# Performance work log

Hardware: AMD Instinct MI355X
Metric: run time of the kernel (lower is better)

Reference implementation:

```python
import jax, jax.numpy as jnp
import numpy as np

K = 3  # n_neighbors


def setup_inputs() -> dict:
    key = jax.random.key(0)
    k1, k2, k3 = jax.random.split(key, 3)
    N, D, C, B = 400000, 27, 11, 512  # train size, 3*N_PEAKS_MAX, classes, query batch
    train_features = jax.random.normal(k1, (N, D), dtype=jnp.float32)
    label_idx = jax.random.randint(k2, (N,), 0, C)
    train_labels = jax.nn.one_hot(label_idx, C, dtype=jnp.float32)
    query = jax.random.normal(k3, (B, D), dtype=jnp.float32)
    return {"query": query, "train_features": train_features, "train_labels": train_labels}


def _divide_no_nan(x, y):
    # tf.math.divide_no_nan: 0 where denominator is 0
    y_safe = jnp.where(y != 0, y, 1.0)
    return jnp.where(y != 0, x / y_safe, 0.0)


def reference(query, train_features, train_labels):
    # scale = per-feature max abs over training set (computed in __init__)
    scale = jnp.max(jnp.abs(train_features), axis=0)            # [D]
    train_s = _divide_no_nan(train_features, scale)             # [N,D]
    q_s = _divide_no_nan(query, scale)                          # [B,D]

    xn = jnp.sum(train_s * train_s, axis=1)                     # [N]
    qn = jnp.sum(q_s * q_s, axis=1)                             # [B]
    d2 = qn[:, None] - 2.0 * jnp.einsum('bd,nd->bn', q_s, train_s) + xn[None, :]
    dist = jnp.sqrt(jnp.maximum(d2, 0.0))                       # [B,N]

    neg_kd, idx = jax.lax.top_k(-dist, K)                       # k smallest distances
    kd = -neg_kd                                                # [B,K]

    lab = train_labels[idx]                                     # [B,K,C]
    # inverse-distance weighted vote (safe against zero distances)
    kd_safe = jnp.where(kd == 0.0, 1.0, kd)
    votes = jnp.sum(lab / kd_safe[:, :, None], axis=1)          # [B,C]
    vote_res = jax.nn.one_hot(jnp.argmax(votes, axis=1), train_labels.shape[1], dtype=jnp.float32)

    # exact-match branch: if the nearest distance is 0, return its label directly
    zero_hit = (jnp.min(kd, axis=1) == 0.0)[:, None]            # [B,1]
    result = jnp.where(zero_hit, lab[:, 0, :], vote_res)        # [B,C]
    return kd, result
```

## Files before the change

### kernel.cpp

```cpp
#include <hip/hip_runtime.h>
#include <math.h>

typedef _Float16 h8 __attribute__((ext_vector_type(8)));
typedef float    f4v __attribute__((ext_vector_type(4)));

#define N_TRAIN 400000
#define DIMS    27
#define BQ      512
#define NCLS    11
#define KNN     3
#define NB      500
#define P1T     1024
#define PTS_BLK 800
#define PTS_SUP 160
#define NSUP    5
#define NPT     10
#define RAWF    4320
#define TILE_B  2048
#define NC      (NB * KNN)
#define SCB     391
#define P2T     512

#define U64MAX 0xFFFFFFFFFFFFFFFFULL

__global__ __launch_bounds__(256) void k_scale(const float* __restrict__ train,
                                               unsigned* __restrict__ scale_u) {
    __shared__ float red[4][DIMS];
    int tid = threadIdx.x;
    int lane = tid & 63, w = tid >> 6;
    int g = blockIdx.x * 256 + tid;
    float m[DIMS];
#pragma unroll
    for (int d = 0; d < DIMS; ++d) m[d] = 0.f;
    if (g < N_TRAIN / 4) {
        const uint4* p = (const uint4*)(train + (size_t)g * (4 * DIMS));
#pragma unroll
        for (int k = 0; k < DIMS; ++k) {
            uint4 v = p[k];
            m[(4 * k + 0) % DIMS] = fmaxf(m[(4 * k + 0) % DIMS], fabsf(__uint_as_float(v.x)));
            m[(4 * k + 1) % DIMS] = fmaxf(m[(4 * k + 1) % DIMS], fabsf(__uint_as_float(v.y)));
            m[(4 * k + 2) % DIMS] = fmaxf(m[(4 * k + 2) % DIMS], fabsf(__uint_as_float(v.z)));
            m[(4 * k + 3) % DIMS] = fmaxf(m[(4 * k + 3) % DIMS], fabsf(__uint_as_float(v.w)));
        }
    }
#pragma unroll
    for (int d = 0; d < DIMS; ++d) {
        float t = m[d];
#pragma unroll
        for (int st = 1; st < 64; st <<= 1) t = fmaxf(t, __shfl_xor(t, st, 64));
        m[d] = t;
    }
    if (lane == 0) {
#pragma unroll
        for (int d = 0; d < DIMS; ++d) red[w][d] = m[d];
    }
    __syncthreads();
    if (tid < DIMS) {
        float v = fmaxf(fmaxf(red[0][tid], red[1][tid]), fmaxf(red[2][tid], red[3][tid]));
        atomicMax(&scale_u[tid], __float_as_uint(v));
    }
}

__device__ __forceinline__ void insert3(float d, int i, float* bd, int* bi) {
    if (d < bd[2] || (d == bd[2] && i < bi[2])) {
        if (d < bd[1] || (d == bd[1] && i < bi[1])) {
            bd[2] = bd[1]; bi[2] = bi[1];
            if (d < bd[0] || (d == bd[0] && i < bi[0])) {
                bd[1] = bd[0]; bi[1] = bi[0];
                bd[0] = d; bi[0] = i;
            } else { bd[1] = d; bi[1] = i; }
        } else { bd[2] = d; bi[2] = i; }
    }
}

__device__ __forceinline__ unsigned long long shfl_xor_u64(unsigned long long v, int m) {
    unsigned lo = (unsigned)v, hi = (unsigned)(v >> 32);
    lo = __shfl_xor(lo, m, 64);
    hi = __shfl_xor(hi, m, 64);
    return ((unsigned long long)hi << 32) | lo;
}

__device__ __forceinline__ void ins3u64(unsigned long long e,
                                        unsigned long long& t0,
                                        unsigned long long& t1,
                                        unsigned long long& t2) {
    unsigned long long a  = e < t2 ? e : t2;
    unsigned long long n2 = t1 > a ? t1 : a;
    unsigned long long n1 = t1 < a ? t1 : a;
    t2 = n2;
    unsigned long long m1 = t0 > n1 ? t0 : n1;
    t0 = t0 < n1 ? t0 : n1;
    t1 = m1;
}

__device__ __forceinline__ void stage16(const float* g, float* l) {
    __builtin_amdgcn_global_load_lds((const __attribute__((address_space(1))) void*)g,
                                     (__attribute__((address_space(3))) void*)l, 16, 0, 0);
}

__global__ __attribute__((amdgpu_flat_work_group_size(P1T, P1T)))
__attribute__((amdgpu_waves_per_eu(4)))
void k_pass1(const float* __restrict__ train,
             const unsigned* __restrict__ scale_u,
             const float* __restrict__ query,
             unsigned long long* __restrict__ cand) {
    __shared__ float s_inv[32];
    __shared__ __align__(16) float raw[2][RAWF];
    __shared__ __align__(16) unsigned char convb[2][NPT * TILE_B];

    int tid = threadIdx.x;
    if (tid < 32) {
        float sc = __uint_as_float(scale_u[tid]);
        s_inv[tid] = (sc != 0.f) ? 1.f / sc : 0.f;
    }
    int lane = tid & 63, w = tid >> 6;
    int l15 = lane & 15, quad = lane >> 4;

    int p0 = blockIdx.x * PTS_BLK;
    const float* gsup = train + (size_t)p0 * DIMS;

    {
        const float* gp = gsup; float* lp = raw[0];
        stage16(gp + tid * 4, lp + tid * 4);
        if (tid < 56) stage16(gp + 4096 + tid * 4, lp + 4096 + tid * 4);
    }

    float iv_[8];
#pragma unroll
    for (int i = 0; i < 8; ++i) {
        int d = quad * 8 + i;
        float sc = __uint_as_float(scale_u[d]);
        iv_[i] = (sc != 0.f) ? 1.f / sc : 0.f;
    }
    h8 bhi[2], blo[2];
#pragma unroll
    for (int j = 0; j < 2; ++j) {
        int q = (w * 2 + j) * 16 + l15;
        const float* qr = query + (size_t)q * DIMS;
#pragma unroll
        for (int i = 0; i < 8; ++i) {
            int d = quad * 8 + i;
            int dc = d < DIMS ? d : (DIMS - 1);
            float xs = qr[dc] * iv_[i];
            _Float16 hi = (_Float16)xs;
            _Float16 lo = (_Float16)(xs - (float)hi);
            bool is27 = (d == 27);
            bhi[j][i] = is27 ? (_Float16)1.f : hi;
            blo[j][i] = is27 ? (_Float16)0.f : lo;
        }
    }

    unsigned kb0[2][4], kb1[2][4];
#pragma unroll
    for (int j = 0; j < 2; ++j)
#pragma unroll
        for (int r = 0; r < 4; ++r) { kb0[j][r] = 0u; kb1[j][r] = 0u; }

    const f4v z4 = {64.f, 64.f, 64.f, 64.f};

    for (int s = 0; s < NSUP; ++s) {
        __syncthreads();

        if (s + 1 < NSUP) {
            const float* gp = gsup + (size_t)(s + 1) * RAWF;
            float* lp = raw[(s + 1) & 1];
            stage16(gp + tid * 4, lp + tid * 4);
            if (tid < 56) stage16(gp + 4096 + tid * 4, lp + 4096 + tid * 4);
        }

        const float* rw = raw[s & 1];
        if (tid < PTS_SUP * 4) {
            int p = tid >> 2, gq = tid & 3;
            float x[8]; float part = 0.f;
#pragma unroll
            for (int i = 0; i < 8; ++i) {
                int d = gq * 8 + i;
                int dc = d < DIMS ? d : (DIMS - 1);
                float v = rw[p * DIMS + dc] * s_inv[d];
                x[i] = v;
                part = fmaf(v, v, part);
            }
            part += __shfl_xor(part, 1, 64);
            part += __shfl_xor(part, 2, 64);
            h8 hv, lv;
#pragma unroll
            for (int i = 0; i < 8; ++i) {
                _Float16 h = (_Float16)x[i];
                hv[i] = h;
                lv[i] = (_Float16)(x[i] - (float)h);
            }
            if (gq == 3) {
                float tt = -0.5f * part;
                _Float16 th = (_Float16)tt;
                hv[3] = th;
                lv[3] = (_Float16)(tt - (float)th);
            }
            unsigned char* dstb = convb[s & 1] + (p >> 4) * TILE_B + gq * 256 + (p & 15) * 16;
            *(h8*)dstb = hv;
            *(h8*)(dstb + 1024) = lv;
        }

        if (s > 0) {
            int ss = s - 1;
            const unsigned char* cb = convb[ss & 1];
            for (int t = 0; t < NPT; ++t) {
                const unsigned char* basep = cb + t * TILE_B;
                h8 ahi = *(const h8*)(basep + lane * 16);
                h8 alo = *(const h8*)(basep + 1024 + lane * 16);
                unsigned ic = 63u - (unsigned)(ss * NPT + t);
#pragma unroll
                for (int j = 0; j < 2; ++j) {
                    f4v acc;
                    acc = __builtin_amdgcn_mfma_f32_16x16x32_f16(alo, bhi[j], z4, 0, 0, 0);
                    acc = __builtin_amdgcn_mfma_f32_16x16x32_f16(ahi, blo[j], acc, 0, 0, 0);
                    acc = __builtin_amdgcn_mfma_f32_16x16x32_f16(ahi, bhi[j], acc, 0, 0, 0);
#pragma unroll
                    for (int r = 0; r < 4; ++r) {
                        unsigned key = (__float_as_uint(acc[r]) & 0xFFFFFFC0u) | ic;
                        unsigned b0 = kb0[j][r];
                        unsigned m  = key < b0 ? key : b0;
                        kb0[j][r]   = key > b0 ? key : b0;
                        unsigned b1 = kb1[j][r];
                        kb1[j][r]   = m > b1 ? m : b1;
                    }
                }
            }
        }
    }

    __syncthreads();
    {
        int ss = NSUP - 1;
        const unsigned char* cb = convb[ss & 1];
        for (int t = 0; t < NPT; ++t) {
            const unsigned char* basep = cb + t * TILE_B;
            h8 ahi = *(const h8*)(basep + lane * 16);
            h8 alo = *(const h8*)(basep + 1024 + lane * 16);
            unsigned ic = 63u - (unsigned)(ss * NPT + t);
#pragma unroll
            for (int j = 0; j < 2; ++j) {
                f4v acc;
                acc = __builtin_amdgcn_mfma_f32_16x16x32_f16(alo, bhi[j], z4, 0, 0, 0);
                acc = __builtin_amdgcn_mfma_f32_16x16x32_f16(ahi, blo[j], acc, 0, 0, 0);
                acc = __builtin_amdgcn_mfma_f32_16x16x32_f16(ahi, bhi[j], acc, 0, 0, 0);
#pragma unroll
                for (int r = 0; r < 4; ++r) {
                    unsigned key = (__float_as_uint(acc[r]) & 0xFFFFFFC0u) | ic;
                    unsigned b0 = kb0[j][r];
                    unsigned m  = key < b0 ? key : b0;
                    kb0[j][r]   = key > b0 ? key : b0;
                    unsigned b1 = kb1[j][r];
                    kb1[j][r]   = m > b1 ? m : b1;
                }
            }
        }
    }

    int g = blockIdx.x;
    int qr4 = quad * 4;
#pragma unroll
    for (int j = 0; j < 2; ++j) {
        unsigned long long t0 = U64MAX, t1 = U64MAX, t2 = U64MAX;
#pragma unroll
        for (int r = 0; r < 4; ++r) {
#pragma unroll
            for (int h = 0; h < 2; ++h) {
                unsigned k = h ? kb1[j][r] : kb0[j][r];
                unsigned tile = 63u - (k & 63u);
                unsigned gi = (unsigned)(p0 + (int)tile * 16 + qr4 + r);
                unsigned long long e = ((unsigned long long)(~(k | 63u)) << 32) | gi;
                ins3u64(e, t0, t1, t2);
            }
        }
#pragma unroll
        for (int step = 16; step <= 32; step <<= 1) {
            unsigned long long o0 = shfl_xor_u64(t0, step);
            unsigned long long o1 = shfl_xor_u64(t1, step);
            unsigned long long o2 = shfl_xor_u64(t2, step);
            ins3u64(o0, t0, t1, t2);
            ins3u64(o1, t0, t1, t2);
            ins3u64(o2, t0, t1, t2);
        }
        if (quad == 0) {
            int qq = (w * 2 + j) * 16 + l15;
            size_t off = (size_t)qq * NC + (size_t)g * KNN;
            cand[off + 0] = t0; cand[off + 1] = t1; cand[off + 2] = t2;
        }
    }
}

#define CE(a, b) do { unsigned long long lo_ = (a) < (b) ? (a) : (b); \
                      unsigned long long hi_ = (a) < (b) ? (b) : (a); \
                      (a) = lo_; (b) = hi_; } while (0)

__global__ __launch_bounds__(P2T) void k_pass2(const unsigned long long* __restrict__ cand,
                                               const float* __restrict__ train,
                                               const float* __restrict__ query,
                                               const unsigned* __restrict__ scale_u,
                                               const float* __restrict__ labels,
                                               float* __restrict__ out) {
    __shared__ unsigned long long smerge[64];
    int q = blockIdx.x;
    int tid = threadIdx.x, lane = tid & 63, w = tid >> 6;
    const unsigned long long* cd = cand + (size_t)q * NC;

    unsigned long long c0 = cd[tid];
    unsigned long long c1 = cd[tid + P2T];
    unsigned long long c2 = (tid + 2 * P2T < NC) ? cd[tid + 2 * P2T] : U64MAX;
    CE(c0, c1); CE(c0, c2); CE(c1, c2);

#pragma unroll
    for (int k = 0; k < 8; ++k) {
        unsigned long long m = c0;
#pragma unroll
        for (int st = 1; st < 64; st <<= 1) {
            unsigned long long o = shfl_xor_u64(m, st);
            if (o < m) m = o;
        }
        if (lane == 0) smerge[w * 8 + k] = m;
        bool win = (c0 == m);
        c0 = win ? c1 : c0;
        c1 = win ? c2 : c1;
        c2 = win ? U64MAX : c2;
    }
    __syncthreads();
    if (w != 0) return;

    int myi = 0x7fffffff;
    {
        unsigned long long cur = smerge[lane];
#pragma unroll
        for (int k = 0; k < 8; ++k) {
            unsigned long long m = cur;
#pragma unroll
            for (int st = 1; st < 64; st <<= 1) {
                unsigned long long o = shfl_xor_u64(m, st);
                if (o < m) m = o;
            }
            if (lane == k) myi = (int)(unsigned)m;
            if (cur == m) cur = U64MAX;
        }
    }

    float inv[DIMS], qs_[DIMS], qn_ = 0.f;
#pragma unroll
    for (int d = 0; d < DIMS; ++d) {
        float sc = __uint_as_float(scale_u[d]);
        float iv = (sc != 0.f) ? 1.f / sc : 0.f;
        float v = query[(size_t)q * DIMS + d] * iv;
        inv[d] = iv; qs_[d] = v;
        qn_ = fmaf(v, v, qn_);
    }

    float myd2 = 3.4e38f;
    if (lane < 8) {
        const float* r = train + (size_t)myi * DIMS;
        float xnv = 0.f, dot = 0.f;
#pragma unroll
        for (int d = 0; d < DIMS; ++d) {
            float v = r[d] * inv[d];
            xnv = fmaf(v, v, xnv);
            dot = fmaf(qs_[d], v, dot);
        }
        myd2 = fmaf(-2.f, dot, qn_ + xnv);
    }

    float bd[KNN] = {3.4e38f, 3.4e38f, 3.4e38f};
    int   bi[KNN] = {0x7fffffff, 0x7fffffff, 0x7fffffff};
#pragma unroll
    for (int k = 0; k < 8; ++k) {
        float dk = __shfl(myd2, k, 64);
        int   ik = __shfl(myi, k, 64);
        insert3(dk, ik, bd, bi);
    }

    if (lane == 0) {
        float kd[KNN];
#pragma unroll
        for (int k = 0; k < KNN; ++k) kd[k] = sqrtf(fmaxf(bd[k], 0.f));
        float lab[KNN][NCLS];
#pragma unroll
        for (int k = 0; k < KNN; ++k) {
            const float* lr = labels + (size_t)bi[k] * NCLS;
#pragma unroll
            for (int c = 0; c < NCLS; ++c) lab[k][c] = lr[c];
        }
        float votes[NCLS];
#pragma unroll
        for (int c = 0; c < NCLS; ++c) votes[c] = 0.f;
#pragma unroll
        for (int k = 0; k < KNN; ++k) {
            float ks = (kd[k] == 0.f) ? 1.f : kd[k];
#pragma unroll
            for (int c = 0; c < NCLS; ++c) votes[c] += lab[k][c] / ks;
        }
        int best = 0; float bv = votes[0];
#pragma unroll
        for (int c = 1; c < NCLS; ++c) { if (votes[c] > bv) { bv = votes[c]; best = c; } }
        bool zero_hit = (kd[0] == 0.f);
#pragma unroll
        for (int k = 0; k < KNN; ++k) out[(size_t)q * KNN + k] = kd[k];
        float* ro = out + (size_t)BQ * KNN + (size_t)q * NCLS;
#pragma unroll
        for (int c = 0; c < NCLS; ++c)
            ro[c] = zero_hit ? lab[0][c] : ((c == best) ? 1.f : 0.f);
    }
}

extern "C" void kernel_launch(void* const* d_in, const int* in_sizes, int n_in,
                              void* d_out, int out_size, void* d_ws, size_t ws_size,
                              hipStream_t stream) {
    const float* query  = (const float*)d_in[0];
    const float* train  = (const float*)d_in[1];
    const float* labels = (const float*)d_in[2];
    float* out = (float*)d_out;

    char* ws = (char*)d_ws;
    unsigned*  scale_u = (unsigned*)ws;
    unsigned long long* cand = (unsigned long long*)(ws + 128);

    hipMemsetAsync(ws, 0, 128, stream);
    k_scale<<<SCB, 256, 0, stream>>>(train, scale_u);
    k_pass1<<<NB, P1T, 0, stream>>>(train, scale_u, query, cand);
    k_pass2<<<BQ, P2T, 0, stream>>>(cand, train, query, scale_u, labels, out);
}
```

Baseline: 176.8 us.

## Fuse scale, candidate and merge passes into one cooperative persistent kernel

Merges the three kernels (scale max, MFMA candidate search, final merge) into a single cooperative launch of 250 blocks that separates phases with grid-wide syncs. Each block now covers twice as many training points. The atomic scale reduction and memset are replaced by per-block partial maxima that every block re-reduces. This removes launch gaps and the memset, at the cost of grid-sync overhead, halved block count for the distance phase, and a redundant scale reduction in each block. A three-kernel fallback runs if the cooperative launch fails.

```diff
diff --git a/kernel.cpp b/kernel.cpp
--- a/kernel.cpp
+++ b/kernel.cpp
@@ -1,5 +1,8 @@
 #include <hip/hip_runtime.h>
+#include <hip/hip_cooperative_groups.h>
 #include <math.h>
+
+namespace cg = cooperative_groups;
 
 typedef _Float16 h8 __attribute__((ext_vector_type(8)));
 typedef float    f4v __attribute__((ext_vector_type(4)));
@@ -9,57 +12,17 @@
 #define BQ      512
 #define NCLS    11
 #define KNN     3
-#define NB      500
+#define NB      250
 #define P1T     1024
-#define PTS_BLK 800
+#define PTS_BLK 1600
 #define PTS_SUP 160
-#define NSUP    5
+#define NSUP    10
 #define NPT     10
 #define RAWF    4320
 #define TILE_B  2048
 #define NC      (NB * KNN)
-#define SCB     391
-#define P2T     512
 
 #define U64MAX 0xFFFFFFFFFFFFFFFFULL
-
-__global__ __launch_bounds__(256) void k_scale(const float* __restrict__ train,
-                                               unsigned* __restrict__ scale_u) {
-    __shared__ float red[4][DIMS];
-    int tid = threadIdx.x;
-    int lane = tid & 63, w = tid >> 6;
-    int g = blockIdx.x * 256 + tid;
-    float m[DIMS];
-#pragma unroll
-    for (int d = 0; d < DIMS; ++d) m[d] = 0.f;
-    if (g < N_TRAIN / 4) {
-        const uint4* p = (const uint4*)(train + (size_t)g * (4 * DIMS));
-#pragma unroll
-        for (int k = 0; k < DIMS; ++k) {
-            uint4 v = p[k];
-            m[(4 * k + 0) % DIMS] = fmaxf(m[(4 * k + 0) % DIMS], fabsf(__uint_as_float(v.x)));
-            m[(4 * k + 1) % DIMS] = fmaxf(m[(4 * k + 1) % DIMS], fabsf(__uint_as_float(v.y)));
-            m[(4 * k + 2) % DIMS] = fmaxf(m[(4 * k + 2) % DIMS], fabsf(__uint_as_float(v.z)));
-            m[(4 * k + 3) % DIMS] = fmaxf(m[(4 * k + 3) % DIMS], fabsf(__uint_as_float(v.w)));
-        }
-    }
-#pragma unroll
-    for (int d = 0; d < DIMS; ++d) {
-        float t = m[d];
-#pragma unroll
-        for (int st = 1; st < 64; st <<= 1) t = fmaxf(t, __shfl_xor(t, st, 64));
-        m[d] = t;
-    }
-    if (lane == 0) {
-#pragma unroll
-        for (int d = 0; d < DIMS; ++d) red[w][d] = m[d];
-    }
-    __syncthreads();
-    if (tid < DIMS) {
-        float v = fmaxf(fmaxf(red[0][tid], red[1][tid]), fmaxf(red[2][tid], red[3][tid]));
-        atomicMax(&scale_u[tid], __float_as_uint(v));
-    }
-}
 
 __device__ __forceinline__ void insert3(float d, int i, float* bd, int* bi) {
     if (d < bd[2] || (d == bd[2] && i < bi[2])) {
@@ -93,45 +56,170 @@
     t1 = m1;
 }
 
+#define CE(a, b) do { unsigned long long lo_ = (a) < (b) ? (a) : (b); \
+                      unsigned long long hi_ = (a) < (b) ? (b) : (a); \
+                      (a) = lo_; (b) = hi_; } while (0)
+
 __device__ __forceinline__ void stage16(const float* g, float* l) {
     __builtin_amdgcn_global_load_lds((const __attribute__((address_space(1))) void*)g,
                                      (__attribute__((address_space(3))) void*)l, 16, 0, 0);
 }
 
-__global__ __attribute__((amdgpu_flat_work_group_size(P1T, P1T)))
-__attribute__((amdgpu_waves_per_eu(4)))
-void k_pass1(const float* __restrict__ train,
-             const unsigned* __restrict__ scale_u,
-             const float* __restrict__ query,
-             unsigned long long* __restrict__ cand) {
-    __shared__ float s_inv[32];
-    __shared__ __align__(16) float raw[2][RAWF];
-    __shared__ __align__(16) unsigned char convb[2][NPT * TILE_B];
-
-    int tid = threadIdx.x;
+__device__ __forceinline__ void phaseS(const float* __restrict__ train,
+                                       float* __restrict__ partial,
+                                       int bid, int tid, float* redS) {
+    int lane = tid & 63, w = tid >> 6;
+    float m[DIMS];
+#pragma unroll
+    for (int d = 0; d < DIMS; ++d) m[d] = 0.f;
+    if (tid < PTS_BLK / 4) {
+        int g = bid * (PTS_BLK / 4) + tid;
+        const uint4* p = (const uint4*)(train + (size_t)g * (4 * DIMS));
+#pragma unroll
+        for (int k = 0; k < DIMS; ++k) {
+            uint4 v = p[k];
+            m[(4 * k + 0) % DIMS] = fmaxf(m[(4 * k + 0) % DIMS], fabsf(__uint_as_float(v.x)));
+            m[(4 * k + 1) % DIMS] = fmaxf(m[(4 * k + 1) % DIMS], fabsf(__uint_as_float(v.y)));
+            m[(4 * k + 2) % DIMS] = fmaxf(m[(4 * k + 2) % DIMS], fabsf(__uint_as_float(v.z)));
+            m[(4 * k + 3) % DIMS] = fmaxf(m[(4 * k + 3) % DIMS], fabsf(__uint_as_float(v.w)));
+        }
+    }
+#pragma unroll
+    for (int d = 0; d < DIMS; ++d) {
+        float t = m[d];
+#pragma unroll
+        for (int st = 1; st < 64; st <<= 1) t = fmaxf(t, __shfl_xor(t, st, 64));
+        m[d] = t;
+    }
+    if (lane == 0) {
+#pragma unroll
+        for (int d = 0; d < DIMS; ++d) redS[w * 32 + d] = m[d];
+    }
+    __syncthreads();
     if (tid < 32) {
-        float sc = __uint_as_float(scale_u[tid]);
+        float v = 0.f;
+        if (tid < DIMS) {
+#pragma unroll
+            for (int g2 = 0; g2 < 16; ++g2) v = fmaxf(v, redS[g2 * 32 + tid]);
+        }
+        partial[bid * 32 + tid] = v;
+    }
+    __threadfence();
+}
+
+__device__ __forceinline__ void scale_reduce(const float* __restrict__ partial,
+                                             float* redP, float* s_inv, int tid) {
+    if (tid < 512) {
+        int d = tid & 31, ch = tid >> 5;
+        float v = 0.f;
+        for (int b = ch; b < NB; b += 16) v = fmaxf(v, partial[b * 32 + d]);
+        redP[ch * 32 + d] = v;
+    }
+    __syncthreads();
+    if (tid < 32) {
+        float sc = 0.f;
+#pragma unroll
+        for (int g2 = 0; g2 < 16; ++g2) sc = fmaxf(sc, redP[g2 * 32 + tid]);
         s_inv[tid] = (sc != 0.f) ? 1.f / sc : 0.f;
     }
+}
+
+__device__ __forceinline__ void conv_tile(const float* rw, unsigned char* dst0,
+                                          int tid, const float* s_inv) {
+    if (tid < PTS_SUP * 4) {
+        int p = tid >> 2, gq = tid & 3;
+        float x[8]; float part = 0.f;
+#pragma unroll
+        for (int i = 0; i < 8; ++i) {
+            int d = gq * 8 + i;
+            int dc = d < DIMS ? d : (DIMS - 1);
+            float v = rw[p * DIMS + dc] * s_inv[d];
+            x[i] = v;
+            part = fmaf(v, v, part);
+        }
+        part += __shfl_xor(part, 1, 64);
+        part += __shfl_xor(part, 2, 64);
+        h8 hv, lv;
+#pragma unroll
+        for (int i = 0; i < 8; ++i) {
+            _Float16 h = (_Float16)x[i];
+            hv[i] = h;
+            lv[i] = (_Float16)(x[i] - (float)h);
+        }
+        if (gq == 3) {
+            float tt = -0.5f * part;
+            _Float16 th = (_Float16)tt;
+            hv[3] = th;
+            lv[3] = (_Float16)(tt - (float)th);
+        }
+        unsigned char* dstb = dst0 + (p >> 4) * TILE_B + gq * 256 + (p & 15) * 16;
+        *(h8*)dstb = hv;
+        *(h8*)(dstb + 1024) = lv;
+    }
+}
+
+__device__ __forceinline__ void compute_super(const unsigned char* cb, int ss, int lane,
+                                              const h8* bhi, const h8* blo,
+                                              unsigned kb0[2][4], unsigned kb1[2][4]) {
+    const f4v z4 = {64.f, 64.f, 64.f, 64.f};
+    for (int t = 0; t < NPT; ++t) {
+        const unsigned char* basep = cb + t * TILE_B;
+        h8 ahi = *(const h8*)(basep + lane * 16);
+        h8 alo = *(const h8*)(basep + 1024 + lane * 16);
+        unsigned ic = 127u - (unsigned)(ss * NPT + t);
+#pragma unroll
+        for (int j = 0; j < 2; ++j) {
+            f4v acc;
+            acc = __builtin_amdgcn_mfma_f32_16x16x32_f16(alo, bhi[j], z4, 0, 0, 0);
+            acc = __builtin_amdgcn_mfma_f32_16x16x32_f16(ahi, blo[j], acc, 0, 0, 0);
+            acc = __builtin_amdgcn_mfma_f32_16x16x32_f16(ahi, bhi[j], acc, 0, 0, 0);
+#pragma unroll
+            for (int r = 0; r < 4; ++r) {
+                unsigned key = (__float_as_uint(acc[r]) & 0xFFFFFF80u) | ic;
+                unsigned b0 = kb0[j][r];
+                unsigned m  = key < b0 ? key : b0;
+                kb0[j][r]   = key > b0 ? key : b0;
+                unsigned b1 = kb1[j][r];
+                kb1[j][r]   = m > b1 ? m : b1;
+            }
+        }
+    }
+}
+
+__device__ __forceinline__ void phaseP1(const float* __restrict__ train,
+                                        const float* __restrict__ query,
+                                        const float* __restrict__ partial,
+                                        unsigned long long* __restrict__ cand,
+                                        int bid, int tid,
+                                        float* s_inv, float* rawb, unsigned char* convbb,
+                                        float* redP) {
     int lane = tid & 63, w = tid >> 6;
     int l15 = lane & 15, quad = lane >> 4;
-
-    int p0 = blockIdx.x * PTS_BLK;
+    int p0 = bid * PTS_BLK;
     const float* gsup = train + (size_t)p0 * DIMS;
 
     {
-        const float* gp = gsup; float* lp = raw[0];
+        const float* gp = gsup; float* lp = rawb;
         stage16(gp + tid * 4, lp + tid * 4);
         if (tid < 56) stage16(gp + 4096 + tid * 4, lp + 4096 + tid * 4);
     }
-
-    float iv_[8];
-#pragma unroll
-    for (int i = 0; i < 8; ++i) {
-        int d = quad * 8 + i;
-        float sc = __uint_as_float(scale_u[d]);
-        iv_[i] = (sc != 0.f) ? 1.f / sc : 0.f;
-    }
+    scale_reduce(partial, redP, s_inv, tid);
+
+    unsigned kb0[2][4], kb1[2][4];
+#pragma unroll
+    for (int j = 0; j < 2; ++j)
+#pragma unroll
+        for (int r = 0; r < 4; ++r) { kb0[j][r] = 0u; kb1[j][r] = 0u; }
+
+    __syncthreads();
+
+    {
+        const float* gp = gsup + RAWF; float* lp = rawb + RAWF;
+        stage16(gp + tid * 4, lp + tid * 4);
+        if (tid < 56) stage16(gp + 4096 + tid * 4, lp + 4096 + tid * 4);
+    }
+    conv_tile(rawb, convbb, tid, s_inv);
+
     h8 bhi[2], blo[2];
 #pragma unroll
     for (int j = 0; j < 2; ++j) {
@@ -141,7 +229,7 @@
         for (int i = 0; i < 8; ++i) {
             int d = quad * 8 + i;
             int dc = d < DIMS ? d : (DIMS - 1);
-            float xs = qr[dc] * iv_[i];
+            float xs = qr[dc] * s_inv[d];
             _Float16 hi = (_Float16)xs;
             _Float16 lo = (_Float16)(xs - (float)hi);
             bool is27 = (d == 27);
@@ -150,113 +238,20 @@
         }
     }
 
-    unsigned kb0[2][4], kb1[2][4];
-#pragma unroll
-    for (int j = 0; j < 2; ++j)
-#pragma unroll
-        for (int r = 0; r < 4; ++r) { kb0[j][r] = 0u; kb1[j][r] = 0u; }
-
-    const f4v z4 = {64.f, 64.f, 64.f, 64.f};
-
-    for (int s = 0; s < NSUP; ++s) {
+    for (int s = 1; s < NSUP; ++s) {
         __syncthreads();
-
         if (s + 1 < NSUP) {
             const float* gp = gsup + (size_t)(s + 1) * RAWF;
-            float* lp = raw[(s + 1) & 1];
+            float* lp = rawb + ((s + 1) & 1) * RAWF;
             stage16(gp + tid * 4, lp + tid * 4);
             if (tid < 56) stage16(gp + 4096 + tid * 4, lp + 4096 + tid * 4);
         }
-
-        const float* rw = raw[s & 1];
-        if (tid < PTS_SUP * 4) {
-            int p = tid >> 2, gq = tid & 3;
-            float x[8]; float part = 0.f;
-#pragma unroll
-            for (int i = 0; i < 8; ++i) {
-                int d = gq * 8 + i;
-                int dc = d < DIMS ? d : (DIMS - 1);
-                float v = rw[p * DIMS + dc] * s_inv[d];
-                x[i] = v;
-                part = fmaf(v, v, part);
-            }
-            part += __shfl_xor(part, 1, 64);
-            part += __shfl_xor(part, 2, 64);
-            h8 hv, lv;
-#pragma unroll
-            for (int i = 0; i < 8; ++i) {
-                _Float16 h = (_Float16)x[i];
-                hv[i] = h;
-                lv[i] = (_Float16)(x[i] - (float)h);
-            }
-            if (gq == 3) {
-                float tt = -0.5f * part;
-                _Float16 th = (_Float16)tt;
-                hv[3] = th;
-                lv[3] = (_Float16)(tt - (float)th);
-            }
-            unsigned char* dstb = convb[s & 1] + (p >> 4) * TILE_B + gq * 256 + (p & 15) * 16;
-            *(h8*)dstb = hv;
-            *(h8*)(dstb + 1024) = lv;
-        }
-
-        if (s > 0) {
-            int ss = s - 1;
-            const unsigned char* cb = convb[ss & 1];
-            for (int t = 0; t < NPT; ++t) {
-                const unsigned char* basep = cb + t * TILE_B;
-                h8 ahi = *(const h8*)(basep + lane * 16);
-                h8 alo = *(const h8*)(basep + 1024 + lane * 16);
-                unsigned ic = 63u - (unsigned)(ss * NPT + t);
-#pragma unroll
-                for (int j = 0; j < 2; ++j) {
-                    f4v acc;
-                    acc = __builtin_amdgcn_mfma_f32_16x16x32_f16(alo, bhi[j], z4, 0, 0, 0);
-                    acc = __builtin_amdgcn_mfma_f32_16x16x32_f16(ahi, blo[j], acc, 0, 0, 0);
-                    acc = __builtin_amdgcn_mfma_f32_16x16x32_f16(ahi, bhi[j], acc, 0, 0, 0);
-#pragma unroll
-                    for (int r = 0; r < 4; ++r) {
-                        unsigned key = (__float_as_uint(acc[r]) & 0xFFFFFFC0u) | ic;
-                        unsigned b0 = kb0[j][r];
-                        unsigned m  = key < b0 ? key : b0;
-                        kb0[j][r]   = key > b0 ? key : b0;
-                        unsigned b1 = kb1[j][r];
-                        kb1[j][r]   = m > b1 ? m : b1;
-                    }
-                }
-            }
-        }
-    }
-
+        conv_tile(rawb + (s & 1) * RAWF, convbb + (s & 1) * (NPT * TILE_B), tid, s_inv);
+        compute_super(convbb + ((s - 1) & 1) * (NPT * TILE_B), s - 1, lane, bhi, blo, kb0, kb1);
+    }
     __syncthreads();
-    {
-        int ss = NSUP - 1;
-        const unsigned char* cb = convb[ss & 1];
-        for (int t = 0; t < NPT; ++t) {
-            const unsigned char* basep = cb + t * TILE_B;
-            h8 ahi = *(const h8*)(basep + lane * 16);
-            h8 alo = *(const h8*)(basep + 1024 + lane * 16);
-            unsigned ic = 63u - (unsigned)(ss * NPT + t);
-#pragma unroll
-            for (int j = 0; j < 2; ++j) {
-                f4v acc;
-                acc = __builtin_amdgcn_mfma_f32_16x16x32_f16(alo, bhi[j], z4, 0, 0, 0);
-                acc = __builtin_amdgcn_mfma_f32_16x16x32_f16(ahi, blo[j], acc, 0, 0, 0);
-                acc = __builtin_amdgcn_mfma_f32_16x16x32_f16(ahi, bhi[j], acc, 0, 0, 0);
-#pragma unroll
-                for (int r = 0; r < 4; ++r) {
-                    unsigned key = (__float_as_uint(acc[r]) & 0xFFFFFFC0u) | ic;
-                    unsigned b0 = kb0[j][r];
-                    unsigned m  = key < b0 ? key : b0;
-                    kb0[j][r]   = key > b0 ? key : b0;
-                    unsigned b1 = kb1[j][r];
-                    kb1[j][r]   = m > b1 ? m : b1;
-                }
-            }
-        }
-    }
-
-    int g = blockIdx.x;
+    compute_super(convbb + ((NSUP - 1) & 1) * (NPT * TILE_B), NSUP - 1, lane, bhi, blo, kb0, kb1);
+
     int qr4 = quad * 4;
 #pragma unroll
     for (int j = 0; j < 2; ++j) {
@@ -266,9 +261,9 @@
 #pragma unroll
             for (int h = 0; h < 2; ++h) {
                 unsigned k = h ? kb1[j][r] : kb0[j][r];
-                unsigned tile = 63u - (k & 63u);
+                unsigned tile = 127u - (k & 127u);
                 unsigned gi = (unsigned)(p0 + (int)tile * 16 + qr4 + r);
-                unsigned long long e = ((unsigned long long)(~(k | 63u)) << 32) | gi;
+                unsigned long long e = ((unsigned long long)(~(k | 127u)) << 32) | gi;
                 ins3u64(e, t0, t1, t2);
             }
         }
@@ -283,128 +278,167 @@
         }
         if (quad == 0) {
             int qq = (w * 2 + j) * 16 + l15;
-            size_t off = (size_t)qq * NC + (size_t)g * KNN;
+            size_t off = (size_t)qq * NC + (size_t)bid * KNN;
             cand[off + 0] = t0; cand[off + 1] = t1; cand[off + 2] = t2;
         }
     }
-}
-
-#define CE(a, b) do { unsigned long long lo_ = (a) < (b) ? (a) : (b); \
-                      unsigned long long hi_ = (a) < (b) ? (b) : (a); \
-                      (a) = lo_; (b) = hi_; } while (0)
-
-__global__ __launch_bounds__(P2T) void k_pass2(const unsigned long long* __restrict__ cand,
-                                               const float* __restrict__ train,
-                                               const float* __restrict__ query,
-                                               const unsigned* __restrict__ scale_u,
-                                               const float* __restrict__ labels,
-                                               float* __restrict__ out) {
-    __shared__ unsigned long long smerge[64];
-    int q = blockIdx.x;
-    int tid = threadIdx.x, lane = tid & 63, w = tid >> 6;
-    const unsigned long long* cd = cand + (size_t)q * NC;
-
-    unsigned long long c0 = cd[tid];
-    unsigned long long c1 = cd[tid + P2T];
-    unsigned long long c2 = (tid + 2 * P2T < NC) ? cd[tid + 2 * P2T] : U64MAX;
-    CE(c0, c1); CE(c0, c2); CE(c1, c2);
-
-#pragma unroll
-    for (int k = 0; k < 8; ++k) {
-        unsigned long long m = c0;
-#pragma unroll
-        for (int st = 1; st < 64; st <<= 1) {
-            unsigned long long o = shfl_xor_u64(m, st);
-            if (o < m) m = o;
-        }
-        if (lane == 0) smerge[w * 8 + k] = m;
-        bool win = (c0 == m);
-        c0 = win ? c1 : c0;
-        c1 = win ? c2 : c1;
-        c2 = win ? U64MAX : c2;
-    }
-    __syncthreads();
-    if (w != 0) return;
-
-    int myi = 0x7fffffff;
-    {
-        unsigned long long cur = smerge[lane];
+    __threadfence();
+}
+
+__device__ __forceinline__ void phaseP2(const unsigned long long* __restrict__ cand,
+                                        const float* __restrict__ train,
+                                        const float* __restrict__ query,
+                                        const float* __restrict__ labels,
+                                        float* __restrict__ out,
+                                        int bid, int tid,
+                                        const float* s_inv, unsigned long long* smerge) {
+    int lane = tid & 63, w = tid >> 6;
+    for (int q = bid; q < BQ; q += NB) {
+        const unsigned long long* cd = cand + (size_t)q * NC;
+        unsigned long long c0 = (tid < NC) ? cd[tid] : U64MAX;
 #pragma unroll
         for (int k = 0; k < 8; ++k) {
-            unsigned long long m = cur;
+            unsigned long long m = c0;
 #pragma unroll
             for (int st = 1; st < 64; st <<= 1) {
                 unsigned long long o = shfl_xor_u64(m, st);
                 if (o < m) m = o;
             }
-            if (lane == k) myi = (int)(unsigned)m;
-            if (cur == m) cur = U64MAX;
-        }
-    }
-
-    float inv[DIMS], qs_[DIMS], qn_ = 0.f;
-#pragma unroll
-    for (int d = 0; d < DIMS; ++d) {
-        float sc = __uint_as_float(scale_u[d]);
-        float iv = (sc != 0.f) ? 1.f / sc : 0.f;
-        float v = query[(size_t)q * DIMS + d] * iv;
-        inv[d] = iv; qs_[d] = v;
-        qn_ = fmaf(v, v, qn_);
-    }
-
-    float myd2 = 3.4e38f;
-    if (lane < 8) {
-        const float* r = train + (size_t)myi * DIMS;
-        float xnv = 0.f, dot = 0.f;
-#pragma unroll
-        for (int d = 0; d < DIMS; ++d) {
-            float v = r[d] * inv[d];
-            xnv = fmaf(v, v, xnv);
-            dot = fmaf(qs_[d], v, dot);
-        }
-        myd2 = fmaf(-2.f, dot, qn_ + xnv);
-    }
-
-    float bd[KNN] = {3.4e38f, 3.4e38f, 3.4e38f};
-    int   bi[KNN] = {0x7fffffff, 0x7fffffff, 0x7fffffff};
-#pragma unroll
-    for (int k = 0; k < 8; ++k) {
-        float dk = __shfl(myd2, k, 64);
-        int   ik = __shfl(myi, k, 64);
-        insert3(dk, ik, bd, bi);
-    }
-
-    if (lane == 0) {
-        float kd[KNN];
-#pragma unroll
-        for (int k = 0; k < KNN; ++k) kd[k] = sqrtf(fmaxf(bd[k], 0.f));
-        float lab[KNN][NCLS];
-#pragma unroll
-        for (int k = 0; k < KNN; ++k) {
-            const float* lr = labels + (size_t)bi[k] * NCLS;
-#pragma unroll
-            for (int c = 0; c < NCLS; ++c) lab[k][c] = lr[c];
-        }
-        float votes[NCLS];
-#pragma unroll
-        for (int c = 0; c < NCLS; ++c) votes[c] = 0.f;
-#pragma unroll
-        for (int k = 0; k < KNN; ++k) {
-            float ks = (kd[k] == 0.f) ? 1.f : kd[k];
-#pragma unroll
-            for (int c = 0; c < NCLS; ++c) votes[c] += lab[k][c] / ks;
-        }
-        int best = 0; float bv = votes[0];
-#pragma unroll
-        for (int c = 1; c < NCLS; ++c) { if (votes[c] > bv) { bv = votes[c]; best = c; } }
-        bool zero_hit = (kd[0] == 0.f);
-#pragma unroll
-        for (int k = 0; k < KNN; ++k) out[(size_t)q * KNN + k] = kd[k];
-        float* ro = out + (size_t)BQ * KNN + (size_t)q * NCLS;
-#pragma unroll
-        for (int c = 0; c < NCLS; ++c)
-            ro[c] = zero_hit ? lab[0][c] : ((c == best) ? 1.f : 0.f);
-    }
+            if (lane == 0) smerge[w * 8 + k] = m;
+            c0 = (c0 == m) ? U64MAX : c0;
+        }
+        __syncthreads();
+
+        if (w == 0) {
+            int myi = 0x7fffffff;
+            unsigned long long e0 = smerge[lane], e1 = smerge[64 + lane];
+            CE(e0, e1);
+#pragma unroll
+            for (int k = 0; k < 8; ++k) {
+                unsigned long long m = e0;
+#pragma unroll
+                for (int st = 1; st < 64; st <<= 1) {
+                    unsigned long long o = shfl_xor_u64(m, st);
+                    if (o < m) m = o;
+                }
+                if (lane == k) myi = (int)(unsigned)m;
+                bool win = (e0 == m);
+                e0 = win ? e1 : e0;
+                e1 = win ? U64MAX : e1;
+            }
+
+            float qn_ = 0.f;
+#pragma unroll
+            for (int d = 0; d < DIMS; ++d) {
+                float v = query[(size_t)q * DIMS + d] * s_inv[d];
+                qn_ = fmaf(v, v, qn_);
+            }
+            float myd2 = 3.4e38f;
+            if (lane < 8) {
+                const float* r = train + (size_t)myi * DIMS;
+                float xnv = 0.f, dot = 0.f;
+#pragma unroll
+                for (int d = 0; d < DIMS; ++d) {
+                    float iv = s_inv[d];
+                    float qv = query[(size_t)q * DIMS + d] * iv;
+                    float tv = r[d] * iv;
+                    xnv = fmaf(tv, tv, xnv);
+                    dot = fmaf(qv, tv, dot);
+                }
+                myd2 = fmaf(-2.f, dot, qn_ + xnv);
+            }
+
+            float bd[KNN] = {3.4e38f, 3.4e38f, 3.4e38f};
+            int   bi[KNN] = {0x7fffffff, 0x7fffffff, 0x7fffffff};
+#pragma unroll
+            for (int k = 0; k < 8; ++k) {
+                float dk = __shfl(myd2, k, 64);
+                int   ik = __shfl(myi, k, 64);
+                insert3(dk, ik, bd, bi);
+            }
+
+            if (lane == 0) {
+                float kd[KNN];
+#pragma unroll
+                for (int k = 0; k < KNN; ++k) kd[k] = sqrtf(fmaxf(bd[k], 0.f));
+                float votes[NCLS];
+#pragma unroll
+                for (int c = 0; c < NCLS; ++c) votes[c] = 0.f;
+#pragma unroll
+                for (int k = 0; k < KNN; ++k) {
+                    float ks = (kd[k] == 0.f) ? 1.f : kd[k];
+                    const float* lr = labels + (size_t)bi[k] * NCLS;
+#pragma unroll
+                    for (int c = 0; c < NCLS; ++c) votes[c] += lr[c] / ks;
+                }
+                int best = 0; float bv = votes[0];
+#pragma unroll
+                for (int c = 1; c < NCLS; ++c) { if (votes[c] > bv) { bv = votes[c]; best = c; } }
+                bool zero_hit = (kd[0] == 0.f);
+#pragma unroll
+                for (int k = 0; k < KNN; ++k) out[(size_t)q * KNN + k] = kd[k];
+                const float* l0 = labels + (size_t)bi[0] * NCLS;
+                float* ro = out + (size_t)BQ * KNN + (size_t)q * NCLS;
+#pragma unroll
+                for (int c = 0; c < NCLS; ++c)
+                    ro[c] = zero_hit ? l0[c] : ((c == best) ? 1.f : 0.f);
+            }
+        }
+        __syncthreads();
+    }
+}
+
+__global__ __attribute__((amdgpu_flat_work_group_size(P1T, P1T)))
+__attribute__((amdgpu_waves_per_eu(4)))
+void k_mega(const float* __restrict__ train,
+            const float* __restrict__ query,
+            const float* __restrict__ labels,
+            float* __restrict__ partial,
+            unsigned long long* __restrict__ cand,
+            float* __restrict__ out) {
+    __shared__ float s_inv[32];
+    __shared__ __align__(16) float raw[2][RAWF];
+    __shared__ __align__(16) unsigned char convb[2][NPT * TILE_B];
+    float* redS = (float*)&convb[0][0];
+    float* redP = (float*)&convb[0][4096];
+    unsigned long long* smerge = (unsigned long long*)&convb[0][8192];
+
+    int tid = threadIdx.x, bid = blockIdx.x;
+    phaseS(train, partial, bid, tid, redS);
+    cg::this_grid().sync();
+    phaseP1(train, query, partial, cand, bid, tid, s_inv, &raw[0][0], &convb[0][0], redP);
+    cg::this_grid().sync();
+    phaseP2(cand, train, query, labels, out, bid, tid, s_inv, smerge);
+}
+
+__global__ __attribute__((amdgpu_flat_work_group_size(P1T, P1T)))
+void k_scale_f(const float* __restrict__ train, float* __restrict__ partial) {
+    __shared__ float redS[16 * 32];
+    phaseS(train, partial, blockIdx.x, threadIdx.x, redS);
+}
+
+__global__ __attribute__((amdgpu_flat_work_group_size(P1T, P1T)))
+__attribute__((amdgpu_waves_per_eu(4)))
+void k_p1_f(const float* __restrict__ train, const float* __restrict__ query,
+            const float* __restrict__ partial, unsigned long long* __restrict__ cand) {
+    __shared__ float s_inv[32];
+    __shared__ __align__(16) float raw[2][RAWF];
+    __shared__ __align__(16) unsigned char convb[2][NPT * TILE_B];
+    float* redP = (float*)&convb[0][4096];
+    phaseP1(train, query, partial, cand, blockIdx.x, threadIdx.x,
+            s_inv, &raw[0][0], &convb[0][0], redP);
+}
+
+__global__ __attribute__((amdgpu_flat_work_group_size(P1T, P1T)))
+void k_p2_f(const unsigned long long* __restrict__ cand, const float* __restrict__ train,
+            const float* __restrict__ query, const float* __restrict__ labels,
+            const float* __restrict__ partial, float* __restrict__ out) {
+    __shared__ float s_inv[32];
+    __shared__ float redP[512];
+    __shared__ unsigned long long smerge[128];
+    scale_reduce(partial, redP, s_inv, threadIdx.x);
+    __syncthreads();
+    phaseP2(cand, train, query, labels, out, blockIdx.x, threadIdx.x, s_inv, smerge);
 }
 
 extern "C" void kernel_launch(void* const* d_in, const int* in_sizes, int n_in,
@@ -416,11 +450,16 @@
     float* out = (float*)d_out;
 
     char* ws = (char*)d_ws;
-    unsigned*  scale_u = (unsigned*)ws;
-    unsigned long long* cand = (unsigned long long*)(ws + 128);
-
-    hipMemsetAsync(ws, 0, 128, stream);
-    k_scale<<<SCB, 256, 0, stream>>>(train, scale_u);
-    k_pass1<<<NB, P1T, 0, stream>>>(train, scale_u, query, cand);
-    k_pass2<<<BQ, P2T, 0, stream>>>(cand, train, query, scale_u, labels, out);
-}
+    float* partial = (float*)ws;
+    unsigned long long* cand = (unsigned long long*)(ws + 32768);
+
+    void* args[] = { (void*)&train, (void*)&query, (void*)&labels,
+                     (void*)&partial, (void*)&cand, (void*)&out };
+    hipError_t err = hipLaunchCooperativeKernel((const void*)k_mega, dim3(NB), dim3(P1T),
+                                                args, 0, stream);
+    if (err != hipSuccess) {
+        k_scale_f<<<NB, P1T, 0, stream>>>(train, partial);
+        k_p1_f<<<NB, P1T, 0, stream>>>(train, query, partial, cand);
+        k_p2_f<<<NB, P1T, 0, stream>>>(cand, train, query, labels, partial, out);
+    }
+}
```

Result: slower. 410.4 us (+132.1%).
